# Performance work log

Measured on AMD Instinct MI355X. Metric: run time of the kernel, lower is better.

Reference implementation:

```python
import jax, jax.numpy as jnp
import numpy as np

HIDDEN = 1024
HEADS = 16
GRAPH_N = 100


def setup_inputs() -> dict:
    key = jax.random.key(0)
    ks = jax.random.split(key, 16)
    B, S, D = 8, 512, HIDDEN
    inp = {
        "v": jax.random.normal(ks[0], (B, S, D), jnp.float32),
        "k": jax.random.normal(ks[1], (B, S, D), jnp.float32),
        "q": jax.random.normal(ks[2], (B, S, D), jnp.float32),
        "mask": jax.random.randint(ks[3], (B, 1, 1, S), 0, 2).astype(bool),
        "graph": jax.random.uniform(ks[4], (B, GRAPH_N, GRAPH_N), jnp.float32),
    }
    s = 1.0 / np.sqrt(D)
    inp["Wv"] = jax.random.normal(ks[5], (D, D), jnp.float32) * s
    inp["bv"] = jnp.zeros((D,), jnp.float32)
    inp["Wk"] = jax.random.normal(ks[6], (D, D), jnp.float32) * s
    inp["bk"] = jnp.zeros((D,), jnp.float32)
    inp["Wq"] = jax.random.normal(ks[7], (D, D), jnp.float32) * s
    inp["bq"] = jnp.zeros((D,), jnp.float32)
    inp["Wm"] = jax.random.normal(ks[8], (D, D), jnp.float32) * s
    inp["bm"] = jnp.zeros((D,), jnp.float32)
    return inp


def _split_heads(x, B, S):
    # (B, S, D) -> (B, H, S, dk)
    return x.reshape(B, S, HEADS, HIDDEN // HEADS).transpose(0, 2, 1, 3)


def reference(v, k, q, mask, graph, Wv, bv, Wk, bk, Wq, bq, Wm, bm):
    B, S, D = q.shape
    dk = D // HEADS

    vh = _split_heads(v @ Wv.T + bv, B, S)
    kh = _split_heads(k @ Wk.T + bk, B, S)
    qh = _split_heads(q @ Wq.T + bq, B, S)

    scores = jnp.einsum("bhqd,bhkd->bhqk", qh, kh) / jnp.sqrt(jnp.float32(dk))

    # graph + I, then (statically) pad to (B, S, S) with ones if S > 100
    g = graph + jnp.eye(GRAPH_N, dtype=graph.dtype)
    if S > GRAPH_N:
        g = jnp.ones((B, S, S), graph.dtype).at[:, :GRAPH_N, :GRAPH_N].set(g)

    causal_scores = scores * g[:, None, :, :]
    causal_scores = jnp.where(mask, jnp.float32(-1e9), causal_scores)
    att = jax.nn.softmax(causal_scores, axis=-1)  # dropout = identity (eval)

    out = jnp.einsum("bhqk,bhkd->bhqd", att, vh)
    out = out.transpose(0, 2, 1, 3).reshape(B, S, D)
    return out @ Wm.T + bm
```

## Files before the change

kernel.cpp:

```cpp
#include <hip/hip_runtime.h>
#include <hip/hip_bf16.h>
#include <math.h>

#define HIDDEN 1024
#define HEADS 16
#define DK 64
#define BB 8
#define SS 512
#define GN 100

typedef __attribute__((ext_vector_type(8))) short short8_t;
typedef __attribute__((ext_vector_type(4))) float f32x4;

__device__ __forceinline__ unsigned short f32_to_bf16_rne(float f) {
  unsigned int u = __float_as_uint(f);
  u += 0x7FFFu + ((u >> 16) & 1u);
  return (unsigned short)(u >> 16);
}
__device__ __forceinline__ float bf16_to_f32(unsigned short h) {
  return __uint_as_float(((unsigned int)h) << 16);
}

typedef const __attribute__((address_space(1))) void* gas_ptr;
typedef __attribute__((address_space(3))) void* las_ptr;
__device__ __forceinline__ void gl16(const void* g, void* l) {
  __builtin_amdgcn_global_load_lds((gas_ptr)g, (las_ptr)l, 16, 0, 0);
}

__global__ __launch_bounds__(256) void round_all(
    const float* __restrict__ s0, const float* __restrict__ s1,
    const float* __restrict__ s2, const float* __restrict__ s3,
    const float* __restrict__ s4, const float* __restrict__ s5,
    const float* __restrict__ s6,
    unsigned short* __restrict__ d0, unsigned short* __restrict__ d1,
    unsigned short* __restrict__ d2, unsigned short* __restrict__ d3,
    unsigned short* __restrict__ d4, unsigned short* __restrict__ d5,
    unsigned short* __restrict__ d6,
    int nBig, int nW) {
  const int z = blockIdx.y;
  const float* src = z == 0 ? s0 : z == 1 ? s1 : z == 2 ? s2 : z == 3 ? s3
                   : z == 4 ? s4 : z == 5 ? s5 : s6;
  unsigned short* dst = z == 0 ? d0 : z == 1 ? d1 : z == 2 ? d2 : z == 3 ? d3
                      : z == 4 ? d4 : z == 5 ? d5 : d6;
  const int n8 = z < 3 ? nBig : nW;
  const int idx = blockIdx.x * 256 + threadIdx.x;
  if (idx >= n8) return;
  const float4* s = (const float4*)src + (size_t)idx * 2;
  const float4 x0 = s[0], x1 = s[1];
  const float xs[8] = {x0.x, x0.y, x0.z, x0.w, x1.x, x1.y, x1.z, x1.w};
  unsigned int p[4];
  #pragma unroll
  for (int i = 0; i < 4; ++i)
    p[i] = (unsigned int)f32_to_bf16_rne(xs[2 * i]) |
           ((unsigned int)f32_to_bf16_rne(xs[2 * i + 1]) << 16);
  uint4 v = {p[0], p[1], p[2], p[3]};
  *((uint4*)dst + idx) = v;
}

__global__ __launch_bounds__(256) void decode_mask_k(
    const unsigned int* __restrict__ raw, unsigned char* __restrict__ outm,
    int n) {
  __shared__ int s_isBytes;
  if (threadIdx.x == 0) s_isBytes = 0;
  __syncthreads();
  int local = 0;
  for (int i = threadIdx.x; i < n / 4; i += 256)
    if (raw[i] > 1u) local = 1;
  if (local) atomicOr(&s_isBytes, 1);
  __syncthreads();
  const int isBytes = s_isBytes;
  for (int i = threadIdx.x; i < n; i += 256) {
    unsigned char v;
    if (isBytes)
      v = (unsigned char)((raw[i >> 2] >> ((i & 3) * 8)) & 0xFFu);
    else
      v = (unsigned char)(raw[i] & 1u);
    outm[i] = v;
  }
}


__global__ __launch_bounds__(256) void gemm_qkv(
    const unsigned short* __restrict__ A0, const unsigned short* __restrict__ A1,
    const unsigned short* __restrict__ A2,
    const unsigned short* __restrict__ B0, const unsigned short* __restrict__ B1,
    const unsigned short* __restrict__ B2,
    const float* __restrict__ bias0, const float* __restrict__ bias1,
    const float* __restrict__ bias2,
    unsigned short* __restrict__ C0, unsigned short* __restrict__ C1,
    unsigned short* __restrict__ C2) {
  __shared__ __align__(16) unsigned short As[128][64];
  __shared__ __align__(16) unsigned short Bs[128][64];

  const int wgid = blockIdx.x;
  const int xcd = wgid & 7, i0 = wgid >> 3;
  const int z = i0 >> 5;
  const int r0 = i0 & 31;
  const int by = xcd * 4 + (r0 >> 3);
  const int bx = r0 & 7;

  const unsigned short* __restrict__ A = z == 0 ? A0 : z == 1 ? A1 : A2;
  const unsigned short* __restrict__ B = z == 0 ? B0 : z == 1 ? B1 : B2;
  const float* __restrict__ bias = z == 0 ? bias0 : z == 1 ? bias1 : bias2;
  unsigned short* __restrict__ C = z == 0 ? C0 : z == 1 ? C1 : C2;

  const int tid = threadIdx.x;
  const int brow0 = by * 128, bcol0 = bx * 128;
  const int w = tid >> 6, l = tid & 63;
  const int wr = w >> 1, wc = w & 1;
  const int l15 = l & 15, l4 = l >> 4;

  f32x4 acc[4][4];
  const f32x4 fzero = {0.f, 0.f, 0.f, 0.f};
  #pragma unroll
  for (int i = 0; i < 4; ++i)
    #pragma unroll
    for (int j = 0; j < 4; ++j) acc[i][j] = fzero;

  const unsigned short* gA = A + (size_t)(brow0 + w * 32 + (l >> 3)) * HIDDEN + (l & 7) * 8;
  const unsigned short* gB = B + (size_t)(bcol0 + w * 32 + (l >> 3)) * HIDDEN + (l & 7) * 8;

  for (int kt = 0; kt < 16; ++kt) {
    const int ko = kt * 64;
    #pragma unroll
    for (int j = 0; j < 4; ++j) {
      gl16(gA + (size_t)j * 8 * HIDDEN + ko, &As[w * 32 + j * 8][0]);
      gl16(gB + (size_t)j * 8 * HIDDEN + ko, &Bs[w * 32 + j * 8][0]);
    }
    __syncthreads();

    #pragma unroll
    for (int s = 0; s < 2; ++s) {
      short8_t af[4], bf[4];
      const int co = s * 32 + l4 * 8;
      #pragma unroll
      for (int i = 0; i < 4; ++i) {
        af[i] = *(const short8_t*)&As[wr * 64 + i * 16 + l15][co];
        bf[i] = *(const short8_t*)&Bs[wc * 64 + i * 16 + l15][co];
      }
      #pragma unroll
      for (int i = 0; i < 4; ++i)
        #pragma unroll
        for (int j = 0; j < 4; ++j)
          acc[i][j] = __builtin_amdgcn_mfma_f32_16x16x32_bf16(af[i], bf[j], acc[i][j], 0, 0, 0);
    }
    __syncthreads();
  }

  unsigned short* cs = &As[0][0];
  #pragma unroll
  for (int i = 0; i < 4; ++i)
    #pragma unroll
    for (int j = 0; j < 4; ++j) {
      const int colL = wc * 64 + j * 16 + l15;
      const float bc = bias[bcol0 + colL];
      #pragma unroll
      for (int r = 0; r < 4; ++r) {
        const int rowL = wr * 64 + i * 16 + l4 * 4 + r;
        cs[rowL * 128 + colL] = f32_to_bf16_rne(acc[i][j][r] + bc);
      }
    }
  __syncthreads();
  #pragma unroll
  for (int t2 = 0; t2 < 8; ++t2) {
    const int rowL = t2 * 16 + (tid >> 4);
    const int colL = (tid & 15) * 8;
    const uint4 val = *(const uint4*)&cs[rowL * 128 + colL];
    *(uint4*)(C + (size_t)(brow0 + rowL) * HIDDEN + bcol0 + colL) = val;
  }
}

__global__ __launch_bounds__(256) void gemm_out(
    const unsigned short* __restrict__ A, const unsigned short* __restrict__ B,
    const float* __restrict__ bias, float* __restrict__ C) {
  __shared__ __align__(16) unsigned short As[128][64];
  __shared__ __align__(16) unsigned short Bs[128][64];

  const int wgid = blockIdx.x;
  const int xcd = wgid & 7, i0 = wgid >> 3;
  const int by = xcd * 4 + (i0 >> 3);
  const int bx = i0 & 7;

  const int tid = threadIdx.x;
  const int brow0 = by * 128, bcol0 = bx * 128;
  const int w = tid >> 6, l = tid & 63;
  const int wr = w >> 1, wc = w & 1;
  const int l15 = l & 15, l4 = l >> 4;

  f32x4 acc[4][4];
  const f32x4 fzero = {0.f, 0.f, 0.f, 0.f};
  #pragma unroll
  for (int i = 0; i < 4; ++i)
    #pragma unroll
    for (int j = 0; j < 4; ++j) acc[i][j] = fzero;

  const unsigned short* gA = A + (size_t)(brow0 + w * 32 + (l >> 3)) * HIDDEN + (l & 7) * 8;
  const unsigned short* gB = B + (size_t)(bcol0 + w * 32 + (l >> 3)) * HIDDEN + (l & 7) * 8;

  for (int kt = 0; kt < 16; ++kt) {
    const int ko = kt * 64;
    #pragma unroll
    for (int j = 0; j < 4; ++j) {
      gl16(gA + (size_t)j * 8 * HIDDEN + ko, &As[w * 32 + j * 8][0]);
      gl16(gB + (size_t)j * 8 * HIDDEN + ko, &Bs[w * 32 + j * 8][0]);
    }
    __syncthreads();

    #pragma unroll
    for (int s = 0; s < 2; ++s) {
      short8_t af[4], bf[4];
      const int co = s * 32 + l4 * 8;
      #pragma unroll
      for (int i = 0; i < 4; ++i) {
        af[i] = *(const short8_t*)&As[wr * 64 + i * 16 + l15][co];
        bf[i] = *(const short8_t*)&Bs[wc * 64 + i * 16 + l15][co];
      }
      #pragma unroll
      for (int i = 0; i < 4; ++i)
        #pragma unroll
        for (int j = 0; j < 4; ++j)
          acc[i][j] = __builtin_amdgcn_mfma_f32_16x16x32_bf16(af[i], bf[j], acc[i][j], 0, 0, 0);
    }
    __syncthreads();
  }

  #pragma unroll
  for (int i = 0; i < 4; ++i)
    #pragma unroll
    for (int j = 0; j < 4; ++j) {
      const int col = bcol0 + wc * 64 + j * 16 + l15;
      const float bc = bias[col];
      #pragma unroll
      for (int r = 0; r < 4; ++r) {
        const int row = brow0 + wr * 64 + i * 16 + l4 * 4 + r;
        C[(size_t)row * HIDDEN + col] = acc[i][j][r] + bc;
      }
    }
}

__global__ __launch_bounds__(256) void vtrans(
    const unsigned short* __restrict__ Vphi, unsigned short* __restrict__ Vthi) {
  __shared__ __align__(16) unsigned short th[64][72];
  const int bh = blockIdx.x;
  const int b = bh >> 4, h = bh & 15;
  const int tid = threadIdx.x;
  const int lr = tid >> 2, lc = tid & 3;
  const int dr = tid >> 2, sq = tid & 3;

  for (int st = 0; st < 8; ++st) {
    const int s0 = st * 64;
    const size_t gi = ((size_t)(b * SS + s0 + lr)) * HIDDEN + h * DK + lc * 16;
    const uint4* ph = (const uint4*)(Vphi + gi);
    *(uint4*)&th[lr][lc * 16] = ph[0];
    *(uint4*)&th[lr][lc * 16 + 8] = ph[1];
    __syncthreads();

    unsigned short oh[16];
    #pragma unroll
    for (int ss = 0; ss < 16; ++ss) oh[ss] = th[sq * 16 + ss][dr];
    const size_t go = ((size_t)(bh * DK + dr)) * SS + s0 + sq * 16;
    *(uint4*)(Vthi + go) = *(uint4*)&oh[0];
    *(uint4*)(Vthi + go + 8) = *(uint4*)&oh[8];
    __syncthreads();
  }
}

#define KP 72

__global__ __launch_bounds__(256) void flash_attn(
    const unsigned short* __restrict__ Qp, const unsigned short* __restrict__ Kp,
    const unsigned short* __restrict__ Vt, const unsigned char* __restrict__ mask,
    const float* __restrict__ graph, unsigned short* __restrict__ Ohi) {
  __shared__ __align__(16) unsigned short Ks[64][KP];
  __shared__ __align__(16) unsigned short Vs[64][KP];
  __shared__ __align__(16) unsigned short Plds[8192];

  const int qt = blockIdx.x, bh = blockIdx.y;
  const int b = bh >> 4, h = bh & 15;
  const int tid = threadIdx.x;
  const int w = tid >> 6, l = tid & 63;
  const int l15 = l & 15, l4 = l >> 4;
  const int qw = w * 32;
  const int q0 = qt * 128;

  short8_t qf[2][2];
  #pragma unroll
  for (int m = 0; m < 2; ++m)
    #pragma unroll
    for (int ks = 0; ks < 2; ++ks)
      qf[m][ks] = *(const short8_t*)(Qp +
          ((size_t)(b * SS + q0 + qw + m * 16 + l15)) * HIDDEN + h * DK + ks * 32 + l4 * 8);

  f32x4 acc[2][4];
  const f32x4 fzero = {0.f, 0.f, 0.f, 0.f};
  #pragma unroll
  for (int m = 0; m < 2; ++m)
    #pragma unroll
    for (int n = 0; n < 4; ++n) acc[m][n] = fzero;
  float rs[2][4] = {};

  const int srow = tid >> 2, sc0 = (tid & 3) * 16;

  for (int kt = 0; kt < 8; ++kt) {
    __syncthreads();
    {
      const unsigned short* ksrc = Kp + ((size_t)(b * SS + kt * 64 + srow)) * HIDDEN + h * DK + sc0;
      *(uint4*)&Ks[srow][sc0]     = *(const uint4*)ksrc;
      *(uint4*)&Ks[srow][sc0 + 8] = *(const uint4*)(ksrc + 8);
      const unsigned short* vsrc = Vt + ((size_t)(bh * DK + srow)) * SS + kt * 64 + sc0;
      *(uint4*)&Vs[srow][sc0]     = *(const uint4*)vsrc;
      *(uint4*)&Vs[srow][sc0 + 8] = *(const uint4*)(vsrc + 8);
    }
    __syncthreads();

    short8_t kf[4][2];
    #pragma unroll
    for (int n = 0; n < 4; ++n)
      #pragma unroll
      for (int ks = 0; ks < 2; ++ks)
        kf[n][ks] = *(const short8_t*)&Ks[n * 16 + l15][ks * 32 + l4 * 8];

    #pragma unroll
    for (int m = 0; m < 2; ++m) {
      #pragma unroll
      for (int n = 0; n < 4; ++n) {
        f32x4 s = fzero;
        s = __builtin_amdgcn_mfma_f32_16x16x32_bf16(qf[m][0], kf[n][0], s, 0, 0, 0);
        s = __builtin_amdgcn_mfma_f32_16x16x32_bf16(qf[m][1], kf[n][1], s, 0, 0, 0);
        const int ki = kt * 64 + n * 16 + l15;
        const bool mj = mask[b * SS + ki] != 0;
        const int kg = (n & 1) * 2 + (l15 >> 3);
        #pragma unroll
        for (int r = 0; r < 4; ++r) {
          float val = s[r] * 0.125f;
          if (qt == 0 && kt < 2) {
            const int qi = qw + m * 16 + l4 * 4 + r;
            if (qi < GN && ki < GN)
              val *= graph[((size_t)b * GN + qi) * GN + ki] + (qi == ki ? 1.0f : 0.0f);
          }
          const float p = mj ? 0.0f : __expf(val - 16.0f);
          rs[m][r] += p;
          const int q = qw + m * 16 + l4 * 4 + r;
          const int idx = (n >> 1) * 4096 + ((q * 4 + (kg ^ ((q >> 2) & 3))) << 3) + (l15 & 7);
          Plds[idx] = f32_to_bf16_rne(p);
        }
      }
    }
    __syncthreads();

    #pragma unroll
    for (int m = 0; m < 2; ++m) {
      const int q = qw + m * 16 + l15;
      #pragma unroll
      for (int ks = 0; ks < 2; ++ks) {
        const short8_t pa = *(const short8_t*)&Plds[ks * 4096 + ((q * 4 + (l4 ^ ((q >> 2) & 3))) << 3)];
        #pragma unroll
        for (int n2 = 0; n2 < 4; ++n2) {
          const short8_t vb = *(const short8_t*)&Vs[n2 * 16 + l15][ks * 32 + l4 * 8];
          acc[m][n2] = __builtin_amdgcn_mfma_f32_16x16x32_bf16(pa, vb, acc[m][n2], 0, 0, 0);
        }
      }
    }
  }

  float inv[2][4];
  #pragma unroll
  for (int m = 0; m < 2; ++m)
    #pragma unroll
    for (int r = 0; r < 4; ++r) {
      float vsum = rs[m][r];
      vsum += __shfl_xor(vsum, 1);
      vsum += __shfl_xor(vsum, 2);
      vsum += __shfl_xor(vsum, 4);
      vsum += __shfl_xor(vsum, 8);
      inv[m][r] = 1.0f / vsum;
    }

  #pragma unroll
  for (int m = 0; m < 2; ++m)
    #pragma unroll
    for (int n2 = 0; n2 < 4; ++n2) {
      const int col = h * DK + n2 * 16 + l15;
      #pragma unroll
      for (int r = 0; r < 4; ++r) {
        const int row = q0 + qw + m * 16 + l4 * 4 + r;
        const float val = acc[m][n2][r] * inv[m][r];
        Ohi[((size_t)(b * SS + row)) * HIDDEN + col] = f32_to_bf16_rne(val);
      }
    }
}

extern "C" void kernel_launch(void* const* d_in, const int* in_sizes, int n_in,
                              void* d_out, int out_size, void* d_ws, size_t ws_size,
                              hipStream_t stream) {
  const float* v     = (const float*)d_in[0];
  const float* k     = (const float*)d_in[1];
  const float* q     = (const float*)d_in[2];
  const unsigned int* mask_raw = (const unsigned int*)d_in[3];
  const float* graph = (const float*)d_in[4];
  const float* Wv = (const float*)d_in[5];
  const float* bv = (const float*)d_in[6];
  const float* Wk = (const float*)d_in[7];
  const float* bk = (const float*)d_in[8];
  const float* Wq = (const float*)d_in[9];
  const float* bq = (const float*)d_in[10];
  const float* Wm = (const float*)d_in[11];
  const float* bm = (const float*)d_in[12];
  float* out = (float*)d_out;

  const size_t MT = (size_t)BB * SS * HIDDEN;
  const size_t WT = (size_t)HIDDEN * HIDDEN;

  char* ws = (char*)d_ws;
  unsigned short* v_bf  = (unsigned short*)ws;  ws += MT * 2;
  unsigned short* k_bf  = (unsigned short*)ws;  ws += MT * 2;
  unsigned short* q_bf  = (unsigned short*)ws;  ws += MT * 2;
  unsigned short* Wv_bf = (unsigned short*)ws;  ws += WT * 2;
  unsigned short* Wk_bf = (unsigned short*)ws;  ws += WT * 2;
  unsigned short* Wq_bf = (unsigned short*)ws;  ws += WT * 2;
  unsigned short* Wm_bf = (unsigned short*)ws;  ws += WT * 2;
  unsigned short* Vp    = (unsigned short*)ws;  ws += MT * 2;
  unsigned short* Kp    = (unsigned short*)ws;  ws += MT * 2;
  unsigned short* Qp    = (unsigned short*)ws;  ws += MT * 2;
  unsigned short* Vt    = (unsigned short*)ws;  ws += MT * 2;
  unsigned char* mask_dec = (unsigned char*)ws; ws += 4096;
  unsigned short* at_bf = v_bf;

  const int nIn8 = (int)(MT / 8);
  const int nW8  = (int)(WT / 8);

  round_all<<<dim3(2048, 7), 256, 0, stream>>>(
      v, k, q, Wv, Wk, Wq, Wm,
      v_bf, k_bf, q_bf, Wv_bf, Wk_bf, Wq_bf, Wm_bf,
      nIn8, nW8);
  decode_mask_k<<<1, 256, 0, stream>>>(mask_raw, mask_dec, BB * SS);

  gemm_qkv<<<dim3(768), 256, 0, stream>>>(
      v_bf, k_bf, q_bf, Wv_bf, Wk_bf, Wq_bf, bv, bk, bq, Vp, Kp, Qp);

  vtrans<<<dim3(BB * HEADS), 256, 0, stream>>>(Vp, Vt);

  flash_attn<<<dim3(SS / 128, BB * HEADS), 256, 0, stream>>>(
      Qp, Kp, Vt, mask_dec, graph, at_bf);

  gemm_out<<<dim3(256), 256, 0, stream>>>(at_bf, Wm_bf, bm, out);
}
```

Baseline: 242.9 us.

## Restructure flash attention with register-prefetched double-buffered K/V and smaller query tiles

```diff
diff --git a/kernel.cpp b/kernel.cpp
--- a/kernel.cpp
+++ b/kernel.cpp
@@ -36,8 +36,31 @@
     unsigned short* __restrict__ d2, unsigned short* __restrict__ d3,
     unsigned short* __restrict__ d4, unsigned short* __restrict__ d5,
     unsigned short* __restrict__ d6,
+    const unsigned int* __restrict__ mask_raw, unsigned char* __restrict__ mask_dec,
     int nBig, int nW) {
   const int z = blockIdx.y;
+  if (z == 7) {
+    if (blockIdx.x != 0) return;
+    __shared__ int s_isBytes;
+    if (threadIdx.x == 0) s_isBytes = 0;
+    __syncthreads();
+    const int n = BB * SS;
+    int local = 0;
+    for (int i = threadIdx.x; i < n / 4; i += 256)
+      if (mask_raw[i] > 1u) local = 1;
+    if (local) atomicOr(&s_isBytes, 1);
+    __syncthreads();
+    const int isBytes = s_isBytes;
+    for (int i = threadIdx.x; i < n; i += 256) {
+      unsigned char v;
+      if (isBytes)
+        v = (unsigned char)((mask_raw[i >> 2] >> ((i & 3) * 8)) & 0xFFu);
+      else
+        v = (unsigned char)(mask_raw[i] & 1u);
+      mask_dec[i] = v;
+    }
+    return;
+  }
   const float* src = z == 0 ? s0 : z == 1 ? s1 : z == 2 ? s2 : z == 3 ? s3
                    : z == 4 ? s4 : z == 5 ? s5 : s6;
   unsigned short* dst = z == 0 ? d0 : z == 1 ? d1 : z == 2 ? d2 : z == 3 ? d3
@@ -57,28 +80,6 @@
   *((uint4*)dst + idx) = v;
 }
 
-__global__ __launch_bounds__(256) void decode_mask_k(
-    const unsigned int* __restrict__ raw, unsigned char* __restrict__ outm,
-    int n) {
-  __shared__ int s_isBytes;
-  if (threadIdx.x == 0) s_isBytes = 0;
-  __syncthreads();
-  int local = 0;
-  for (int i = threadIdx.x; i < n / 4; i += 256)
-    if (raw[i] > 1u) local = 1;
-  if (local) atomicOr(&s_isBytes, 1);
-  __syncthreads();
-  const int isBytes = s_isBytes;
-  for (int i = threadIdx.x; i < n; i += 256) {
-    unsigned char v;
-    if (isBytes)
-      v = (unsigned char)((raw[i >> 2] >> ((i & 3) * 8)) & 0xFFu);
-    else
-      v = (unsigned char)(raw[i] & 1u);
-    outm[i] = v;
-  }
-}
-
 
 __global__ __launch_bounds__(256) void gemm_qkv(
     const unsigned short* __restrict__ A0, const unsigned short* __restrict__ A1,
@@ -265,129 +266,135 @@
   }
 }
 
-#define KP 72
-
 __global__ __launch_bounds__(256) void flash_attn(
     const unsigned short* __restrict__ Qp, const unsigned short* __restrict__ Kp,
     const unsigned short* __restrict__ Vt, const unsigned char* __restrict__ mask,
     const float* __restrict__ graph, unsigned short* __restrict__ Ohi) {
-  __shared__ __align__(16) unsigned short Ks[64][KP];
-  __shared__ __align__(16) unsigned short Vs[64][KP];
-  __shared__ __align__(16) unsigned short Plds[8192];
+  __shared__ __align__(16) unsigned short Ks[2][64][64];
+  __shared__ __align__(16) unsigned short Vs[2][64][64];
+  __shared__ __align__(16) unsigned short Plds[4096];
 
   const int qt = blockIdx.x, bh = blockIdx.y;
   const int b = bh >> 4, h = bh & 15;
   const int tid = threadIdx.x;
   const int w = tid >> 6, l = tid & 63;
   const int l15 = l & 15, l4 = l >> 4;
-  const int qw = w * 32;
-  const int q0 = qt * 128;
-
-  short8_t qf[2][2];
-  #pragma unroll
-  for (int m = 0; m < 2; ++m)
-    #pragma unroll
-    for (int ks = 0; ks < 2; ++ks)
-      qf[m][ks] = *(const short8_t*)(Qp +
-          ((size_t)(b * SS + q0 + qw + m * 16 + l15)) * HIDDEN + h * DK + ks * 32 + l4 * 8);
-
-  f32x4 acc[2][4];
+  const int qw = w * 16;
+  const int q0 = qt * 64;
+
+  short8_t qf[2];
+  #pragma unroll
+  for (int ks = 0; ks < 2; ++ks)
+    qf[ks] = *(const short8_t*)(Qp +
+        ((size_t)(b * SS + q0 + qw + l15)) * HIDDEN + h * DK + ks * 32 + l4 * 8);
+
+  f32x4 acc[4];
   const f32x4 fzero = {0.f, 0.f, 0.f, 0.f};
   #pragma unroll
-  for (int m = 0; m < 2; ++m)
-    #pragma unroll
-    for (int n = 0; n < 4; ++n) acc[m][n] = fzero;
-  float rs[2][4] = {};
-
-  const int srow = tid >> 2, sc0 = (tid & 3) * 16;
-
-  for (int kt = 0; kt < 8; ++kt) {
-    __syncthreads();
+  for (int n = 0; n < 4; ++n) acc[n] = fzero;
+  float rs[4] = {};
+
+  const int srow = tid >> 2;
+  const int sslot = (tid & 3) * 2;
+  const unsigned short* kg0 = Kp + ((size_t)(b * SS + srow)) * HIDDEN + h * DK + sslot * 8;
+  const unsigned short* vg0 = Vt + ((size_t)(bh * DK + srow)) * SS + sslot * 8;
+  const int sw0 = (sslot ^ (srow & 7)) * 8;
+  const int sw1 = ((sslot + 1) ^ (srow & 7)) * 8;
+
+  uint4 kr0 = *(const uint4*)kg0, kr1 = *(const uint4*)(kg0 + 8);
+  uint4 vr0 = *(const uint4*)vg0, vr1 = *(const uint4*)(vg0 + 8);
+
+  int p = 0;
+  for (int kt = 0; kt < 8; ++kt, p ^= 1) {
+    *(uint4*)&Ks[p][srow][sw0] = kr0;
+    *(uint4*)&Ks[p][srow][sw1] = kr1;
+    *(uint4*)&Vs[p][srow][sw0] = vr0;
+    *(uint4*)&Vs[p][srow][sw1] = vr1;
+    __syncthreads();
+
+    if (kt < 7) {
+      const unsigned short* kg = kg0 + (size_t)(kt + 1) * 64 * HIDDEN;
+      const unsigned short* vg = vg0 + (kt + 1) * 64;
+      kr0 = *(const uint4*)kg; kr1 = *(const uint4*)(kg + 8);
+      vr0 = *(const uint4*)vg; vr1 = *(const uint4*)(vg + 8);
+    }
+
+    f32x4 sc[4];
+    __builtin_amdgcn_s_setprio(1);
+    #pragma unroll
+    for (int n = 0; n < 4; ++n) {
+      f32x4 s = fzero;
+      #pragma unroll
+      for (int ks = 0; ks < 2; ++ks) {
+        const short8_t kf = *(const short8_t*)
+            &Ks[p][n * 16 + l15][((ks * 4 + l4) ^ (l15 & 7)) * 8];
+        s = __builtin_amdgcn_mfma_f32_16x16x32_bf16(qf[ks], kf, s, 0, 0, 0);
+      }
+      sc[n] = s;
+    }
+    __builtin_amdgcn_s_setprio(0);
+
+    #pragma unroll
+    for (int n = 0; n < 4; ++n) {
+      const int ki = kt * 64 + n * 16 + l15;
+      const bool mj = mask[b * SS + ki] != 0;
+      const int kg_ = (n & 1) * 2 + (l15 >> 3);
+      #pragma unroll
+      for (int r = 0; r < 4; ++r) {
+        float val = sc[n][r] * 0.125f;
+        if (q0 < GN && kt < 2) {
+          const int qi = q0 + qw + l4 * 4 + r;
+          if (qi < GN && ki < GN)
+            val *= graph[((size_t)b * GN + qi) * GN + ki] + (qi == ki ? 1.0f : 0.0f);
+        }
+        const float pv = mj ? 0.0f : __expf(val - 16.0f);
+        rs[r] += pv;
+        const int q = qw + l4 * 4 + r;
+        const int idx = (n >> 1) * 2048 + ((q * 4 + (kg_ ^ ((q >> 2) & 3))) << 3) + (l15 & 7);
+        Plds[idx] = f32_to_bf16_rne(pv);
+      }
+    }
+    __syncthreads();
+
+    __builtin_amdgcn_s_setprio(1);
     {
-      const unsigned short* ksrc = Kp + ((size_t)(b * SS + kt * 64 + srow)) * HIDDEN + h * DK + sc0;
-      *(uint4*)&Ks[srow][sc0]     = *(const uint4*)ksrc;
-      *(uint4*)&Ks[srow][sc0 + 8] = *(const uint4*)(ksrc + 8);
-      const unsigned short* vsrc = Vt + ((size_t)(bh * DK + srow)) * SS + kt * 64 + sc0;
-      *(uint4*)&Vs[srow][sc0]     = *(const uint4*)vsrc;
-      *(uint4*)&Vs[srow][sc0 + 8] = *(const uint4*)(vsrc + 8);
-    }
-    __syncthreads();
-
-    short8_t kf[4][2];
-    #pragma unroll
-    for (int n = 0; n < 4; ++n)
-      #pragma unroll
-      for (int ks = 0; ks < 2; ++ks)
-        kf[n][ks] = *(const short8_t*)&Ks[n * 16 + l15][ks * 32 + l4 * 8];
-
-    #pragma unroll
-    for (int m = 0; m < 2; ++m) {
-      #pragma unroll
-      for (int n = 0; n < 4; ++n) {
-        f32x4 s = fzero;
-        s = __builtin_amdgcn_mfma_f32_16x16x32_bf16(qf[m][0], kf[n][0], s, 0, 0, 0);
-        s = __builtin_amdgcn_mfma_f32_16x16x32_bf16(qf[m][1], kf[n][1], s, 0, 0, 0);
-        const int ki = kt * 64 + n * 16 + l15;
-        const bool mj = mask[b * SS + ki] != 0;
-        const int kg = (n & 1) * 2 + (l15 >> 3);
-        #pragma unroll
-        for (int r = 0; r < 4; ++r) {
-          float val = s[r] * 0.125f;
-          if (qt == 0 && kt < 2) {
-            const int qi = qw + m * 16 + l4 * 4 + r;
-            if (qi < GN && ki < GN)
-              val *= graph[((size_t)b * GN + qi) * GN + ki] + (qi == ki ? 1.0f : 0.0f);
-          }
-          const float p = mj ? 0.0f : __expf(val - 16.0f);
-          rs[m][r] += p;
-          const int q = qw + m * 16 + l4 * 4 + r;
-          const int idx = (n >> 1) * 4096 + ((q * 4 + (kg ^ ((q >> 2) & 3))) << 3) + (l15 & 7);
-          Plds[idx] = f32_to_bf16_rne(p);
-        }
-      }
-    }
-    __syncthreads();
-
-    #pragma unroll
-    for (int m = 0; m < 2; ++m) {
-      const int q = qw + m * 16 + l15;
+      const int q = qw + l15;
       #pragma unroll
       for (int ks = 0; ks < 2; ++ks) {
-        const short8_t pa = *(const short8_t*)&Plds[ks * 4096 + ((q * 4 + (l4 ^ ((q >> 2) & 3))) << 3)];
+        const short8_t pa = *(const short8_t*)
+            &Plds[ks * 2048 + ((q * 4 + (l4 ^ ((q >> 2) & 3))) << 3)];
         #pragma unroll
         for (int n2 = 0; n2 < 4; ++n2) {
-          const short8_t vb = *(const short8_t*)&Vs[n2 * 16 + l15][ks * 32 + l4 * 8];
-          acc[m][n2] = __builtin_amdgcn_mfma_f32_16x16x32_bf16(pa, vb, acc[m][n2], 0, 0, 0);
+          const short8_t vb = *(const short8_t*)
+              &Vs[p][n2 * 16 + l15][((ks * 4 + l4) ^ (l15 & 7)) * 8];
+          acc[n2] = __builtin_amdgcn_mfma_f32_16x16x32_bf16(pa, vb, acc[n2], 0, 0, 0);
         }
       }
     }
-  }
-
-  float inv[2][4];
-  #pragma unroll
-  for (int m = 0; m < 2; ++m)
+    __builtin_amdgcn_s_setprio(0);
+  }
+
+  float inv[4];
+  #pragma unroll
+  for (int r = 0; r < 4; ++r) {
+    float vsum = rs[r];
+    vsum += __shfl_xor(vsum, 1);
+    vsum += __shfl_xor(vsum, 2);
+    vsum += __shfl_xor(vsum, 4);
+    vsum += __shfl_xor(vsum, 8);
+    inv[r] = 1.0f / vsum;
+  }
+
+  #pragma unroll
+  for (int n2 = 0; n2 < 4; ++n2) {
+    const int col = h * DK + n2 * 16 + l15;
     #pragma unroll
     for (int r = 0; r < 4; ++r) {
-      float vsum = rs[m][r];
-      vsum += __shfl_xor(vsum, 1);
-      vsum += __shfl_xor(vsum, 2);
-      vsum += __shfl_xor(vsum, 4);
-      vsum += __shfl_xor(vsum, 8);
-      inv[m][r] = 1.0f / vsum;
-    }
-
-  #pragma unroll
-  for (int m = 0; m < 2; ++m)
-    #pragma unroll
-    for (int n2 = 0; n2 < 4; ++n2) {
-      const int col = h * DK + n2 * 16 + l15;
-      #pragma unroll
-      for (int r = 0; r < 4; ++r) {
-        const int row = q0 + qw + m * 16 + l4 * 4 + r;
-        const float val = acc[m][n2][r] * inv[m][r];
-        Ohi[((size_t)(b * SS + row)) * HIDDEN + col] = f32_to_bf16_rne(val);
-      }
-    }
+      const int row = q0 + qw + l4 * 4 + r;
+      const float val = acc[n2][r] * inv[r];
+      Ohi[((size_t)(b * SS + row)) * HIDDEN + col] = f32_to_bf16_rne(val);
+    }
+  }
 }
 
 extern "C" void kernel_launch(void* const* d_in, const int* in_sizes, int n_in,
@@ -429,18 +436,17 @@
   const int nIn8 = (int)(MT / 8);
   const int nW8  = (int)(WT / 8);
 
-  round_all<<<dim3(2048, 7), 256, 0, stream>>>(
+  round_all<<<dim3(2048, 8), 256, 0, stream>>>(
       v, k, q, Wv, Wk, Wq, Wm,
       v_bf, k_bf, q_bf, Wv_bf, Wk_bf, Wq_bf, Wm_bf,
-      nIn8, nW8);
-  decode_mask_k<<<1, 256, 0, stream>>>(mask_raw, mask_dec, BB * SS);
+      mask_raw, mask_dec, nIn8, nW8);
 
   gemm_qkv<<<dim3(768), 256, 0, stream>>>(
       v_bf, k_bf, q_bf, Wv_bf, Wk_bf, Wq_bf, bv, bk, bq, Vp, Kp, Qp);
 
   vtrans<<<dim3(BB * HEADS), 256, 0, stream>>>(Vp, Vt);
 
-  flash_attn<<<dim3(SS / 128, BB * HEADS), 256, 0, stream>>>(
+  flash_attn<<<dim3(SS / 64, BB * HEADS), 256, 0, stream>>>(
       Qp, Kp, Vt, mask_dec, graph, at_bf);
 
   gemm_out<<<dim3(256), 256, 0, stream>>>(at_bf, Wm_bf, bm, out);
```

Result: faster. 231.2 us (-4.8%).
